# Performance work log

Hardware: AMD Instinct MI355X
Metric: run time of the kernel (lower is better)

## Reference

```python
import jax, jax.numpy as jnp
import numpy as np

BLOCK_K = 32   # BLOCK_K_SIZE_MIN in the original Triton kernel
BLOCK_N = 32   # output-block granularity of the hash


def _hash_indices(random_numbers, num_nb, num_kb, num_red_kb):
    # universal hash of (n_block, k_block) -> reduced k-block index
    r = random_numbers.astype(jnp.uint32)
    nb = jnp.arange(num_nb, dtype=jnp.uint32)[:, None]
    kb = jnp.arange(num_kb, dtype=jnp.uint32)[None, :]
    hv = (kb * r[0] + nb * r[1] + r[2]) ^ r[3]
    return (hv % jnp.uint32(num_red_kb)).astype(jnp.int32)  # [num_nb, num_kb]


def _ssl_forward(x, weight, bias, random_numbers):
    orig_shape = x.shape
    K = orig_shape[-1]
    x2 = x.reshape(-1, K)                       # [M, K]
    N, red_K = weight.shape
    num_kb = K // BLOCK_K
    num_red_kb = red_K // BLOCK_K
    num_nb = N // BLOCK_N
    h = _hash_indices(random_numbers, num_nb, num_kb, num_red_kb)  # [num_nb, num_kb]
    # Gather the virtual full weight from the reduced weight via hash indices.
    wb = weight.reshape(num_nb, BLOCK_N, num_red_kb, BLOCK_K)
    w_full = jnp.take_along_axis(wb, h[:, None, :, None], axis=2)  # [num_nb, BN, num_kb, BK]
    w_full = w_full.reshape(N, K)
    y = x2 @ w_full.T
    if bias is not None:
        y = y + bias
    return y.reshape(*orig_shape[:-1], N)


def setup_inputs() -> dict:
    key = jax.random.key(0)
    k1, k2, k3 = jax.random.split(key, 3)
    in_features, out_features, redn_factor, seed = 8192, 512, 8, 1024
    red_in = ((in_features // redn_factor + BLOCK_K - 1) // BLOCK_K) * BLOCK_K  # 1024
    x = jax.random.normal(k1, (4, 2048, in_features), dtype=jnp.float32)
    bound = 1.0 / np.sqrt(red_in)
    weight = jax.random.uniform(k2, (out_features, red_in), jnp.float32, -bound, bound)
    bias = jax.random.uniform(k3, (out_features,), jnp.float32, -bound, bound)
    rng = np.random.default_rng(seed)
    random_numbers = jnp.asarray(rng.integers(1, 2**31 - 1, size=4), dtype=jnp.int32)
    return {"x": x, "weight": weight, "bias": bias,
            "random_numbers": random_numbers, "redn_factor": redn_factor}


def reference(x, weight, bias, random_numbers, redn_factor):
    return _ssl_forward(x, weight, bias, random_numbers)
```

## Files before the change

### kernel.cpp

```cpp
#include <hip/hip_runtime.h>
#include <hip/hip_bf16.h>
#include <stdint.h>


typedef __bf16 bf16x4_t __attribute__((ext_vector_type(4)));
typedef __bf16 bf16x8_t __attribute__((ext_vector_type(8)));
typedef float f32x4 __attribute__((ext_vector_type(4)));

#define BM 128
#define BN 128
#define BK 32

__global__ __launch_bounds__(256, 1) void ssl_gemm(
    const float* __restrict__ X,
    const float* __restrict__ W,
    const float* __restrict__ Bias,
    const int* __restrict__ RN,
    float* __restrict__ Out,
    int M, int N, int K, int redK, uint32_t numRedKb, int mTiles) {
  __shared__ __align__(16) __bf16 As[BM * BK];
  __shared__ __align__(16) __bf16 Bs[BN * BK];

  const uint32_t r0 = (uint32_t)RN[0], r1 = (uint32_t)RN[1];
  const uint32_t r2 = (uint32_t)RN[2], r3 = (uint32_t)RN[3];
  const uint32_t redMask = numRedKb - 1u;
  const bool pow2 = (numRedKb & (numRedKb - 1u)) == 0u;

  const int id = blockIdx.x;
  const int mTile = id % mTiles;
  const int nTile = id / mTiles;

  const int tid = threadIdx.x;
  const int wave = tid >> 6;
  const int lane = tid & 63;
  const int wm = wave >> 1, wn = wave & 1;

  const int lRow = tid >> 3;
  const int lCol = (tid & 7) << 2;
  const float* aBase = X + (size_t)(mTile * BM + lRow) * K + lCol;
  const float* bBase = W + (size_t)(nTile * BN + lRow) * redK + lCol;

  auto loadA = [&](int kb, f32x4* r) {
    const float* p = aBase + (size_t)kb * BK;
#pragma unroll
    for (int i = 0; i < 4; ++i)
      r[i] = *(const f32x4*)(p + (size_t)(i * 32) * K);
  };
  auto loadB = [&](int kb, f32x4* r) {
    const uint32_t kk = (uint32_t)kb * r0 + r2;
#pragma unroll
    for (int i = 0; i < 4; ++i) {
      const uint32_t nb = (uint32_t)(nTile * (BN / 32) + i);
      const uint32_t hv = (kk + nb * r1) ^ r3;
      const uint32_t h = pow2 ? (hv & redMask) : (hv % numRedKb);
      r[i] = *(const f32x4*)(bBase + (size_t)(i * 32) * redK + h * 32u);
    }
  };
  auto stage = [&](const f32x4* rA, const f32x4* rB) {
#pragma unroll
    for (int i = 0; i < 4; ++i) {
      bf16x4_t a, b;
#pragma unroll
      for (int j = 0; j < 4; ++j) {
        a[j] = (__bf16)rA[i][j];
        b[j] = (__bf16)rB[i][j];
      }
      *(bf16x4_t*)&As[(i * 32 + lRow) * BK + lCol] = a;
      *(bf16x4_t*)&Bs[(i * 32 + lRow) * BK + lCol] = b;
    }
  };

  f32x4 acc[4][4] = {};
  auto compute = [&]() {
    bf16x8_t af[4], bfr[4];
    const int kOff = (lane >> 4) << 3;
    const int r16 = lane & 15;
#pragma unroll
    for (int mi = 0; mi < 4; ++mi)
      af[mi] = *(const bf16x8_t*)&As[((wm << 6) + (mi << 4) + r16) * BK + kOff];
#pragma unroll
    for (int ni = 0; ni < 4; ++ni)
      bfr[ni] = *(const bf16x8_t*)&Bs[((wn << 6) + (ni << 4) + r16) * BK + kOff];
#pragma unroll
    for (int mi = 0; mi < 4; ++mi)
#pragma unroll
      for (int ni = 0; ni < 4; ++ni)
        acc[mi][ni] = __builtin_amdgcn_mfma_f32_16x16x32_bf16(
            af[mi], bfr[ni], acc[mi][ni], 0, 0, 0);
  };

  const int numKb = K / BK;
  f32x4 a0[4], b0[4], a1[4], b1[4];
  loadA(0, a0);
  loadB(0, b0);
  for (int kb = 0; kb < numKb; kb += 2) {
    if (kb + 1 < numKb) { loadA(kb + 1, a1); loadB(kb + 1, b1); }
    __syncthreads();
    stage(a0, b0);
    __syncthreads();
    compute();
    if (kb + 2 < numKb) { loadA(kb + 2, a0); loadB(kb + 2, b0); }
    __syncthreads();
    stage(a1, b1);
    __syncthreads();
    compute();
  }

  const int mBase = mTile * BM + (wm << 6);
  const int nBase = nTile * BN + (wn << 6);
#pragma unroll
  for (int ni = 0; ni < 4; ++ni) {
    const int n = nBase + (ni << 4) + (lane & 15);
    const float bv = Bias[n];
#pragma unroll
    for (int mi = 0; mi < 4; ++mi) {
      const int m0 = mBase + (mi << 4) + ((lane >> 4) << 2);
#pragma unroll
      for (int r = 0; r < 4; ++r)
        Out[(size_t)(m0 + r) * N + n] = acc[mi][ni][r] + bv;
    }
  }
}

extern "C" void kernel_launch(void* const* d_in, const int* in_sizes, int n_in,
                              void* d_out, int out_size, void* d_ws, size_t ws_size,
                              hipStream_t stream) {
  const float* X = (const float*)d_in[0];
  const float* W = (const float*)d_in[1];
  const float* Bias = (const float*)d_in[2];
  const int* RN = (const int*)d_in[3];
  float* Out = (float*)d_out;

  const int N = in_sizes[2];
  const int M = out_size / N;
  const int K = in_sizes[0] / M;
  const int redK = in_sizes[1] / N;
  const uint32_t numRedKb = (uint32_t)(redK / 32);

  const int mTiles = M / BM;
  const int nTiles = N / BN;
  dim3 grid(mTiles * nTiles), block(256);
  ssl_gemm<<<grid, block, 0, stream>>>(X, W, Bias, RN, Out,
                                       M, N, K, redK, numRedKb, mTiles);
}
```

Measured before the change: 551.5 us.

## Split K across blocks with atomic accumulation and pad LDS rows

Splits the K dimension into four chunks so the grid grows from 256 to 1024 blocks, giving more parallelism across the GPU's compute units. A new kernel pre-fills the output with the bias, and each split block atomically adds its partial sums. LDS rows are also padded from 32 to 40 bf16 elements to cut bank conflicts on the fragment reads. The cost is an extra init kernel, four times as many fp32 atomics to global memory, and run-to-run nondeterministic summation order.

```diff
diff --git a/kernel.cpp b/kernel.cpp
--- a/kernel.cpp
+++ b/kernel.cpp
@@ -10,16 +10,27 @@
 #define BM 128
 #define BN 128
 #define BK 32
+#define LDSK 40
+#define KSPLIT 4
+
+__global__ void init_out(float* __restrict__ Out, const float* __restrict__ Bias,
+                         int N, int total4) {
+  int i = blockIdx.x * blockDim.x + threadIdx.x;
+  if (i < total4) {
+    int idx = i << 2;
+    int n = idx % N;
+    *(f32x4*)(Out + idx) = *(const f32x4*)(Bias + n);
+  }
+}
 
 __global__ __launch_bounds__(256, 1) void ssl_gemm(
     const float* __restrict__ X,
     const float* __restrict__ W,
-    const float* __restrict__ Bias,
     const int* __restrict__ RN,
     float* __restrict__ Out,
-    int M, int N, int K, int redK, uint32_t numRedKb, int mTiles) {
-  __shared__ __align__(16) __bf16 As[BM * BK];
-  __shared__ __align__(16) __bf16 Bs[BN * BK];
+    int M, int N, int K, int redK, uint32_t numRedKb, int mTiles, int nTiles) {
+  __shared__ __align__(16) __bf16 As[BM * LDSK];
+  __shared__ __align__(16) __bf16 Bs[BN * LDSK];
 
   const uint32_t r0 = (uint32_t)RN[0], r1 = (uint32_t)RN[1];
   const uint32_t r2 = (uint32_t)RN[2], r3 = (uint32_t)RN[3];
@@ -28,7 +39,9 @@
 
   const int id = blockIdx.x;
   const int mTile = id % mTiles;
-  const int nTile = id / mTiles;
+  const int rest = id / mTiles;
+  const int nTile = rest % nTiles;
+  const int kChunk = rest / nTiles;
 
   const int tid = threadIdx.x;
   const int wave = tid >> 6;
@@ -65,8 +78,8 @@
         a[j] = (__bf16)rA[i][j];
         b[j] = (__bf16)rB[i][j];
       }
-      *(bf16x4_t*)&As[(i * 32 + lRow) * BK + lCol] = a;
-      *(bf16x4_t*)&Bs[(i * 32 + lRow) * BK + lCol] = b;
+      *(bf16x4_t*)&As[(i * 32 + lRow) * LDSK + lCol] = a;
+      *(bf16x4_t*)&Bs[(i * 32 + lRow) * LDSK + lCol] = b;
     }
   };
 
@@ -77,10 +90,10 @@
     const int r16 = lane & 15;
 #pragma unroll
     for (int mi = 0; mi < 4; ++mi)
-      af[mi] = *(const bf16x8_t*)&As[((wm << 6) + (mi << 4) + r16) * BK + kOff];
+      af[mi] = *(const bf16x8_t*)&As[((wm << 6) + (mi << 4) + r16) * LDSK + kOff];
 #pragma unroll
     for (int ni = 0; ni < 4; ++ni)
-      bfr[ni] = *(const bf16x8_t*)&Bs[((wn << 6) + (ni << 4) + r16) * BK + kOff];
+      bfr[ni] = *(const bf16x8_t*)&Bs[((wn << 6) + (ni << 4) + r16) * LDSK + kOff];
 #pragma unroll
     for (int mi = 0; mi < 4; ++mi)
 #pragma unroll
@@ -90,16 +103,18 @@
   };
 
   const int numKb = K / BK;
+  const int kbN = numKb / KSPLIT;
+  const int kb0 = kChunk * kbN;
   f32x4 a0[4], b0[4], a1[4], b1[4];
-  loadA(0, a0);
-  loadB(0, b0);
-  for (int kb = 0; kb < numKb; kb += 2) {
-    if (kb + 1 < numKb) { loadA(kb + 1, a1); loadB(kb + 1, b1); }
+  loadA(kb0, a0);
+  loadB(kb0, b0);
+  for (int i = 0; i < kbN; i += 2) {
+    if (i + 1 < kbN) { loadA(kb0 + i + 1, a1); loadB(kb0 + i + 1, b1); }
     __syncthreads();
     stage(a0, b0);
     __syncthreads();
     compute();
-    if (kb + 2 < numKb) { loadA(kb + 2, a0); loadB(kb + 2, b0); }
+    if (i + 2 < kbN) { loadA(kb0 + i + 2, a0); loadB(kb0 + i + 2, b0); }
     __syncthreads();
     stage(a1, b1);
     __syncthreads();
@@ -111,13 +126,12 @@
 #pragma unroll
   for (int ni = 0; ni < 4; ++ni) {
     const int n = nBase + (ni << 4) + (lane & 15);
-    const float bv = Bias[n];
 #pragma unroll
     for (int mi = 0; mi < 4; ++mi) {
       const int m0 = mBase + (mi << 4) + ((lane >> 4) << 2);
 #pragma unroll
       for (int r = 0; r < 4; ++r)
-        Out[(size_t)(m0 + r) * N + n] = acc[mi][ni][r] + bv;
+        unsafeAtomicAdd(&Out[(size_t)(m0 + r) * N + n], acc[mi][ni][r]);
     }
   }
 }
@@ -137,9 +151,12 @@
   const int redK = in_sizes[1] / N;
   const uint32_t numRedKb = (uint32_t)(redK / 32);
 
+  const int total4 = out_size / 4;
+  init_out<<<(total4 + 255) / 256, 256, 0, stream>>>(Out, Bias, N, total4);
+
   const int mTiles = M / BM;
   const int nTiles = N / BN;
-  dim3 grid(mTiles * nTiles), block(256);
-  ssl_gemm<<<grid, block, 0, stream>>>(X, W, Bias, RN, Out,
-                                       M, N, K, redK, numRedKb, mTiles);
+  dim3 grid(mTiles * nTiles * KSPLIT), block(256);
+  ssl_gemm<<<grid, block, 0, stream>>>(X, W, RN, Out,
+                                       M, N, K, redK, numRedKb, mTiles, nTiles);
 }
```

Measured after the change: 504.1 us. 8.6% less time.
